# Kernel optimization log

Hardware: AMD Instinct MI355X
Metric: run time of the kernel (lower is better)

The kernel has to match this reference:

```python
import jax, jax.numpy as jnp
import numpy as np

B, D, T, K = 32, 64, 4096, 512
COMMITMENT_COST = 0.25


def setup_inputs() -> dict:
    key = jax.random.key(0)
    k1, k2 = jax.random.split(key)
    z = jax.random.normal(k1, (B, D, T), dtype=jnp.float32)
    # nn.Embedding init: uniform(-1/K, 1/K)
    codebook = jax.random.uniform(k2, (K, D), dtype=jnp.float32,
                                  minval=-1.0 / K, maxval=1.0 / K)
    return {"z": z, "codebook": codebook}


def reference(z, codebook):
    sg = jax.lax.stop_gradient
    zt = jnp.transpose(z, (0, 2, 1))            # [B, T, D]
    zf = zt.reshape(-1, D)                      # [N, D], N = B*T
    # squared L2 distances: ||z||^2 + ||e||^2 - 2 z.e  -> [N, K]
    dists = (jnp.sum(zf * zf, axis=1, keepdims=True)
             + jnp.sum(codebook * codebook, axis=1)
             - 2.0 * jnp.matmul(zf, codebook.T))
    idx = jnp.argmin(dists, axis=1)             # [N]
    # gather codebook rows (same math as one-hot @ codebook)
    quantized = codebook[idx].reshape(zt.shape)  # [B, T, D]
    codebook_loss = jnp.mean((sg(quantized) - zt) ** 2)
    commitment_loss = jnp.mean((quantized - sg(zt)) ** 2)
    vq_loss = codebook_loss + COMMITMENT_COST * commitment_loss
    # straight-through estimator
    quantized_st = zt + sg(quantized - zt)
    quantized_out = jnp.transpose(quantized_st, (0, 2, 1))  # [B, D, T]
    indices = idx.reshape(B, T)
    return vq_loss, quantized_out, indices
```

## Files before the change

### kernel.cpp

```cpp
#include <hip/hip_runtime.h>

#define NB 32
#define ND 64
#define NT 4096
#define NK 512
#define NGRID 1024

typedef __attribute__((ext_vector_type(8))) short short8;
typedef __attribute__((ext_vector_type(16))) float f32x16;
typedef unsigned int uint32;
typedef unsigned short ushort16_t;

#define PERM(r) ((((r) & 7) * 16) + ((r) >> 3))
#define STR 68
#define ESTR 66
#define MARGIN 4e-4f
#define RCAP 4

__device__ __forceinline__ ushort16_t bf16rne(float f) {
    uint32 u = __float_as_uint(f);
    return (ushort16_t)((u + 0x7FFFu + ((u >> 16) & 1u)) >> 16);
}
__device__ __forceinline__ float bf16tof(ushort16_t h) {
    return __uint_as_float(((uint32)h) << 16);
}

__global__ void prep_kernel(const float* __restrict__ cb,
                            uint4* __restrict__ cbfrag,
                            float* __restrict__ enorm,
                            double* __restrict__ loss_acc,
                            uint32* __restrict__ counter) {
    const int bi = blockIdx.x, tid = threadIdx.x;
    if (bi < 16) {
        const int t = bi * 256 + tid;
        const int c = t >> 8, rem = t & 255, s = rem >> 6, L = rem & 63;
        const int kcode = c * 32 + (L & 31);
        const int dbase = s * 16 + ((L >> 5) << 3);
        const float* src = cb + (size_t)kcode * 64 + dbase;
        const float4 pa = *(const float4*)src;
        const float4 pb = *(const float4*)(src + 4);
        const float f[8] = {pa.x, pa.y, pa.z, pa.w, pb.x, pb.y, pb.z, pb.w};
        uint32 hw[4], lw[4];
#pragma unroll
        for (int i = 0; i < 4; ++i) {
            const ushort16_t h0 = bf16rne(f[2*i]);
            const ushort16_t h1 = bf16rne(f[2*i+1]);
            const ushort16_t l0 = bf16rne(f[2*i]   - bf16tof(h0));
            const ushort16_t l1 = bf16rne(f[2*i+1] - bf16tof(h1));
            hw[i] = (uint32)h0 | ((uint32)h1 << 16);
            lw[i] = (uint32)l0 | ((uint32)l1 << 16);
        }
        cbfrag[(size_t)((c*4+s)*2 + 0)*64 + L] = make_uint4(hw[0],hw[1],hw[2],hw[3]);
        cbfrag[(size_t)((c*4+s)*2 + 1)*64 + L] = make_uint4(lw[0],lw[1],lw[2],lw[3]);
    } else {
        if (tid == 0) { *loss_acc = 0.0; *counter = 0u; }
        for (int k = tid; k < NK; k += 256) {
            const float* e = cb + (size_t)k * ND;
            float r[8];
#pragma unroll
            for (int j = 0; j < 8; ++j) {
                float s = __fmul_rn(e[j], e[j]);
#pragma unroll
                for (int i = 1; i < 8; ++i)
                    s = __fadd_rn(s, __fmul_rn(e[8*i+j], e[8*i+j]));
                r[j] = s;
            }
            enorm[k] = __fadd_rn(__fadd_rn(__fadd_rn(r[0],r[1]), __fadd_rn(r[2],r[3])),
                                 __fadd_rn(__fadd_rn(r[4],r[5]), __fadd_rn(r[6],r[7])));
        }
    }
}

__device__ __forceinline__ float exact_dist(const float* __restrict__ zrow,
                                            const float* __restrict__ cb,
                                            const float* __restrict__ enl,
                                            float zn, int k2) {
    const float4* e4 = (const float4*)(cb + (size_t)k2 * ND);
    float a = 0.0f;
#pragma unroll
    for (int w = 0; w < 16; ++w) {
        const float4 ev = e4[w];
        const float4 zv = *(const float4*)(zrow + 4 * w);
        a = __builtin_fmaf(zv.x, ev.x, a);
        a = __builtin_fmaf(zv.y, ev.y, a);
        a = __builtin_fmaf(zv.z, ev.z, a);
        a = __builtin_fmaf(zv.w, ev.w, a);
    }
    return __fsub_rn(__fadd_rn(zn, enl[k2]), __fmul_rn(2.0f, a));
}

__global__ __launch_bounds__(256, 3) void vq_main(const float* __restrict__ z,
                                                  const float* __restrict__ cb,
                                                  const uint4* __restrict__ cbfrag,
                                                  const float* __restrict__ enorm,
                                                  float* __restrict__ qout,
                                                  float* __restrict__ idxout,
                                                  double* __restrict__ loss_acc,
                                                  uint32* __restrict__ counter,
                                                  float* __restrict__ out0) {
    __shared__ __align__(16) char smem[46112];
    float*       zl   = (float*)smem;
    float*       enl  = (float*)(smem + 34816);
    float*       znl  = (float*)(smem + 36864);
    ushort16_t*  cand = (ushort16_t*)(smem + 37376);
    int*         sfin = (int*)(smem + 45568);
    double*      sred = (double*)(smem + 46080);

    const int bi    = blockIdx.x;
    const int b     = bi >> 5;
    const int tbase = (bi & 31) * 128;
    const int tid   = threadIdx.x;
    const size_t zoff = (size_t)b * (ND * NT) + tbase;

#pragma unroll
    for (int j = 0; j < 8; ++j) {
        const int qq = j * 256 + tid;
        const int i4 = qq & 31, d = qq >> 5;
        const float4 v = *(const float4*)(z + zoff + (size_t)d * NT + i4 * 4);
        const float vv[4] = {v.x, v.y, v.z, v.w};
#pragma unroll
        for (int c = 0; c < 4; ++c) {
            const int r = i4 * 4 + c;
            zl[PERM(r) * STR + d] = vv[c];
        }
    }
    for (int k = tid; k < NK; k += 256) enl[k] = enorm[k];
    __syncthreads();

    if (tid < 128) {
        const int r = tid;
        const float4* zr4 = (const float4*)&zl[PERM(r) * STR];
        float x[64];
#pragma unroll
        for (int wq = 0; wq < 16; ++wq) {
            const float4 t4 = zr4[wq];
            x[4*wq] = t4.x; x[4*wq+1] = t4.y; x[4*wq+2] = t4.z; x[4*wq+3] = t4.w;
        }
        float r8[8];
#pragma unroll
        for (int jj = 0; jj < 8; ++jj) {
            float s = __fmul_rn(x[jj], x[jj]);
#pragma unroll
            for (int ii = 1; ii < 8; ++ii)
                s = __fadd_rn(s, __fmul_rn(x[8*ii+jj], x[8*ii+jj]));
            r8[jj] = s;
        }
        znl[r] = __fadd_rn(__fadd_rn(__fadd_rn(r8[0],r8[1]), __fadd_rn(r8[2],r8[3])),
                           __fadd_rn(__fadd_rn(r8[4],r8[5]), __fadd_rn(r8[6],r8[7])));
    }

    const int L    = tid & 63;
    const int w    = tid >> 6;
    const int h    = L >> 5;
    const int rowl = w * 32 + (L & 31);
    short8 bhf[4], blf[4];
    {
        const float* zrow = &zl[PERM(rowl) * STR];
#pragma unroll
        for (int s = 0; s < 4; ++s) {
            const int d0 = s * 16 + h * 8;
            const float4 pa = *(const float4*)(zrow + d0);
            const float4 pb = *(const float4*)(zrow + d0 + 4);
            const float f[8] = {pa.x, pa.y, pa.z, pa.w, pb.x, pb.y, pb.z, pb.w};
            uint32 hw[4], lw[4];
#pragma unroll
            for (int i = 0; i < 4; ++i) {
                const ushort16_t h0 = bf16rne(f[2*i]);
                const ushort16_t h1 = bf16rne(f[2*i+1]);
                const ushort16_t l0 = bf16rne(f[2*i]   - bf16tof(h0));
                const ushort16_t l1 = bf16rne(f[2*i+1] - bf16tof(h1));
                hw[i] = (uint32)h0 | ((uint32)h1 << 16);
                lw[i] = (uint32)l0 | ((uint32)l1 << 16);
            }
            union { uint4 u; short8 s8; } uh, ul;
            uh.u = make_uint4(hw[0],hw[1],hw[2],hw[3]);
            ul.u = make_uint4(lw[0],lw[1],lw[2],lw[3]);
            bhf[s] = uh.s8; blf[s] = ul.s8;
        }
    }
    __syncthreads();

    float best  = __builtin_inff();
    int   bestk = 0;
    {
        uint4 buf0[8], buf1[8];
#pragma unroll
        for (int p = 0; p < 8; ++p) buf0[p] = cbfrag[(size_t)p * 64 + L];
#pragma unroll 2
        for (int c = 0; c < 16; ++c) {
            const uint4* cur = (c & 1) ? buf1 : buf0;
            uint4*       nxt = (c & 1) ? buf0 : buf1;
#pragma unroll
            for (int p = 0; p < 8; ++p)
                nxt[p] = cbfrag[(size_t)((c + 1) * 8 + p) * 64 + L];
            f32x16 acc;
#pragma unroll
            for (int r = 0; r < 16; ++r) acc[r] = 0.0f;
#pragma unroll
            for (int s = 0; s < 4; ++s) {
                union { uint4 u; short8 s8; } ah, al;
                ah.u = cur[s * 2 + 0];
                al.u = cur[s * 2 + 1];
                acc = __builtin_amdgcn_mfma_f32_32x32x16_bf16(ah.s8, bhf[s], acc, 0, 0, 0);
                acc = __builtin_amdgcn_mfma_f32_32x32x16_bf16(al.s8, bhf[s], acc, 0, 0, 0);
                acc = __builtin_amdgcn_mfma_f32_32x32x16_bf16(ah.s8, blf[s], acc, 0, 0, 0);
            }
#pragma unroll
            for (int r = 0; r < 16; ++r) {
                const int kc = c * 32 + ((r & 3) + 8 * (r >> 2) + 4 * h);
                const float sv = __builtin_fmaf(-2.0f, acc[r], enl[kc]);
                if (sv < best) { best = sv; bestk = kc; }
            }
        }
    }
    {
        const float ob  = __shfl_xor(best, 32);
        const int   obk = __shfl_xor(bestk, 32);
        if (ob < best || (ob == best && obk < bestk)) { best = ob; bestk = obk; }
    }
    const float thresh = best + MARGIN;

    int myc = 0, ovf = 0;
    ushort16_t* mylist = cand + (rowl * 2 + h) * RCAP;
    {
        uint4 buf0[8], buf1[8];
#pragma unroll
        for (int p = 0; p < 8; ++p) buf0[p] = cbfrag[(size_t)p * 64 + L];
#pragma unroll 2
        for (int c = 0; c < 16; ++c) {
            const uint4* cur = (c & 1) ? buf1 : buf0;
            uint4*       nxt = (c & 1) ? buf0 : buf1;
#pragma unroll
            for (int p = 0; p < 8; ++p)
                nxt[p] = cbfrag[(size_t)((c + 1) * 8 + p) * 64 + L];
            f32x16 acc;
#pragma unroll
            for (int r = 0; r < 16; ++r) acc[r] = 0.0f;
#pragma unroll
            for (int s = 0; s < 4; ++s) {
                union { uint4 u; short8 s8; } ah, al;
                ah.u = cur[s * 2 + 0];
                al.u = cur[s * 2 + 1];
                acc = __builtin_amdgcn_mfma_f32_32x32x16_bf16(ah.s8, bhf[s], acc, 0, 0, 0);
                acc = __builtin_amdgcn_mfma_f32_32x32x16_bf16(al.s8, bhf[s], acc, 0, 0, 0);
                acc = __builtin_amdgcn_mfma_f32_32x32x16_bf16(ah.s8, blf[s], acc, 0, 0, 0);
            }
#pragma unroll
            for (int r = 0; r < 16; ++r) {
                const int kc = c * 32 + ((r & 3) + 8 * (r >> 2) + 4 * h);
                const float sv = __builtin_fmaf(-2.0f, acc[r], enl[kc]);
                if (sv <= thresh && kc != bestk) {
                    if (myc < RCAP) mylist[myc++] = (ushort16_t)kc;
                    else ovf = 1;
                }
            }
        }
    }

    const float* zrow = &zl[PERM(rowl) * STR];
    const float  zn   = znl[rowl];
    const int    totr = myc + __shfl_xor(myc, 32);
    const int    aovf = ovf | __shfl_xor(ovf, 32);

    int bk;
    if (aovf) {
        float bd = __builtin_inff(); bk = 0x7FFFFFFF;
        for (int c = 0; c < 16; ++c)
#pragma unroll
            for (int qd = 0; qd < 4; ++qd)
#pragma unroll
                for (int i = 0; i < 4; ++i) {
                    const int k2 = c * 32 + qd * 8 + h * 4 + i;
                    const float dv = exact_dist(zrow, cb, enl, zn, k2);
                    if (dv < bd || (dv == bd && k2 < bk)) { bd = dv; bk = k2; }
                }
        const float obd = __shfl_xor(bd, 32);
        const int   obk = __shfl_xor(bk, 32);
        if (obd < bd || (obd == bd && obk < bk)) bk = obk;
    } else if (totr > 0) {
        float bd = __builtin_inff(); bk = 0x7FFFFFFF;
        if (((bestk >> 2) & 1) == h) {
            bd = exact_dist(zrow, cb, enl, zn, bestk);
            bk = bestk;
        }
        for (int i = 0; i < myc; ++i) {
            const int k2 = mylist[i];
            const float dv = exact_dist(zrow, cb, enl, zn, k2);
            if (dv < bd || (dv == bd && k2 < bk)) { bd = dv; bk = k2; }
        }
        const float obd = __shfl_xor(bd, 32);
        const int   obk = __shfl_xor(bk, 32);
        if (obd < bd || (obd == bd && obk < bk)) bk = obk;
    } else {
        bk = bestk;
    }
    if (h == 0) {
        sfin[rowl] = bk;
        idxout[(size_t)b * NT + tbase + rowl] = (float)bk;
    }
    __syncthreads();

    float* ech = zl;
#pragma unroll
    for (int j = 0; j < 8; ++j) {
        const int qq  = j * 256 + tid;
        const int row = qq >> 4, d4 = qq & 15;
        const float4 v = *(const float4*)(cb + (size_t)sfin[row] * ND + d4 * 4);
        float* dst = &ech[row * ESTR + d4 * 4];
        *(float2*)(dst)     = make_float2(v.x, v.y);
        *(float2*)(dst + 2) = make_float2(v.z, v.w);
    }
    __syncthreads();

    double lsum = 0.0;
#pragma unroll 4
    for (int j = 0; j < 32; ++j) {
        const int qq = j * 256 + tid;
        const int ir = qq & 127, d = qq >> 7;
        const float zv = z[zoff + (size_t)d * NT + ir];
        const float ev = ech[ir * ESTR + d];
        const float diff = __fsub_rn(ev, zv);
        qout[(size_t)b * (ND*NT) + (size_t)d * NT + tbase + ir] = __fadd_rn(zv, diff);
        lsum += (double)diff * (double)diff;
    }
#pragma unroll
    for (int off = 32; off > 0; off >>= 1) lsum += __shfl_down(lsum, off, 64);
    if ((tid & 63) == 0) sred[tid >> 6] = lsum;
    __syncthreads();

    if (tid == 0) {
        const double bsum = (sred[0] + sred[1]) + (sred[2] + sred[3]);
        atomicAdd(loss_acc, bsum);
        __threadfence();
        const uint32 old = atomicAdd(counter, 1u);
        if (old == (uint32)(NGRID - 1)) {
            __threadfence();
            const double tot = *(volatile double*)loss_acc;
            const double m = tot / (double)((size_t)NB * NT * ND);
            out0[0] = (float)(1.25 * m);
        }
    }
}

extern "C" void kernel_launch(void* const* d_in, const int* in_sizes, int n_in,
                              void* d_out, int out_size, void* d_ws, size_t ws_size,
                              hipStream_t stream) {
    const float* z  = (const float*)d_in[0];
    const float* cb = (const float*)d_in[1];

    float* out      = (float*)d_out;
    float* loss_out = out;
    float* qout     = out + 1;
    float* idxout   = out + 1 + (size_t)NB * ND * NT;

    uint4*  cbfrag   = (uint4*)d_ws;
    float*  enorm    = (float*)((char*)d_ws + 139264);
    double* loss_acc = (double*)((char*)d_ws + 141312);
    uint32* counter  = (uint32*)((char*)d_ws + 141320);

    prep_kernel<<<17, 256, 0, stream>>>(cb, cbfrag, enorm, loss_acc, counter);
    vq_main<<<NGRID, 256, 0, stream>>>(z, cb, cbfrag, enorm, qout, idxout,
                                       loss_acc, counter, loss_out);
}
```

Measured before the change: 201.1 us.

## Fuse candidate collection into single MFMA pass with register ring buffer

Removes the second full MFMA distance pass over the codebook. Near-best candidates are now tracked in a single pass, packed as quantized scores plus indices into a four-entry register shift buffer. This drops the shared-memory candidate list, shrinking LDS so launch bounds can target 4 blocks per SM. The cost is more branchy per-element logic, extra register pressure, and a possibly different overflow pattern that falls back to the exact full scan.

```diff
diff --git a/kernel.cpp b/kernel.cpp
--- a/kernel.cpp
+++ b/kernel.cpp
@@ -14,8 +14,7 @@
 #define PERM(r) ((((r) & 7) * 16) + ((r) >> 3))
 #define STR 68
 #define ESTR 66
-#define MARGIN 4e-4f
-#define RCAP 4
+#define M2 4e-4f
 
 __device__ __forceinline__ ushort16_t bf16rne(float f) {
     uint32 u = __float_as_uint(f);
@@ -89,7 +88,7 @@
     return __fsub_rn(__fadd_rn(zn, enl[k2]), __fmul_rn(2.0f, a));
 }
 
-__global__ __launch_bounds__(256, 3) void vq_main(const float* __restrict__ z,
+__global__ __launch_bounds__(256, 4) void vq_main(const float* __restrict__ z,
                                                   const float* __restrict__ cb,
                                                   const uint4* __restrict__ cbfrag,
                                                   const float* __restrict__ enorm,
@@ -98,13 +97,12 @@
                                                   double* __restrict__ loss_acc,
                                                   uint32* __restrict__ counter,
                                                   float* __restrict__ out0) {
-    __shared__ __align__(16) char smem[46112];
+    __shared__ __align__(16) char smem[37920];
     float*       zl   = (float*)smem;
     float*       enl  = (float*)(smem + 34816);
     float*       znl  = (float*)(smem + 36864);
-    ushort16_t*  cand = (ushort16_t*)(smem + 37376);
-    int*         sfin = (int*)(smem + 45568);
-    double*      sred = (double*)(smem + 46080);
+    int*         sfin = (int*)(smem + 37376);
+    double*      sred = (double*)(smem + 37888);
 
     const int bi    = blockIdx.x;
     const int b     = bi >> 5;
@@ -180,8 +178,12 @@
     }
     __syncthreads();
 
-    float best  = __builtin_inff();
-    int   bestk = 0;
+    float  bmax = -__builtin_inff();
+    int    bk   = 0;
+    float  thr  = -__builtin_inff();
+    uint32 thrq = 0xFFFFFFFFu;
+    uint32 r0 = 0u, r1 = 0u, r2 = 0u, r3 = 0u;
+    int    ovf  = 0;
     {
         uint4 buf0[8], buf1[8];
 #pragma unroll
@@ -207,64 +209,53 @@
             }
 #pragma unroll
             for (int r = 0; r < 16; ++r) {
-                const int kc = c * 32 + ((r & 3) + 8 * (r >> 2) + 4 * h);
-                const float sv = __builtin_fmaf(-2.0f, acc[r], enl[kc]);
-                if (sv < best) { best = sv; bestk = kc; }
-            }
-        }
-    }
-    {
-        const float ob  = __shfl_xor(best, 32);
-        const int   obk = __shfl_xor(bestk, 32);
-        if (ob < best || (ob == best && obk < bestk)) { best = ob; bestk = obk; }
-    }
-    const float thresh = best + MARGIN;
-
-    int myc = 0, ovf = 0;
-    ushort16_t* mylist = cand + (rowl * 2 + h) * RCAP;
-    {
-        uint4 buf0[8], buf1[8];
-#pragma unroll
-        for (int p = 0; p < 8; ++p) buf0[p] = cbfrag[(size_t)p * 64 + L];
-#pragma unroll 2
-        for (int c = 0; c < 16; ++c) {
-            const uint4* cur = (c & 1) ? buf1 : buf0;
-            uint4*       nxt = (c & 1) ? buf0 : buf1;
-#pragma unroll
-            for (int p = 0; p < 8; ++p)
-                nxt[p] = cbfrag[(size_t)((c + 1) * 8 + p) * 64 + L];
-            f32x16 acc;
-#pragma unroll
-            for (int r = 0; r < 16; ++r) acc[r] = 0.0f;
-#pragma unroll
-            for (int s = 0; s < 4; ++s) {
-                union { uint4 u; short8 s8; } ah, al;
-                ah.u = cur[s * 2 + 0];
-                al.u = cur[s * 2 + 1];
-                acc = __builtin_amdgcn_mfma_f32_32x32x16_bf16(ah.s8, bhf[s], acc, 0, 0, 0);
-                acc = __builtin_amdgcn_mfma_f32_32x32x16_bf16(al.s8, bhf[s], acc, 0, 0, 0);
-                acc = __builtin_amdgcn_mfma_f32_32x32x16_bf16(ah.s8, blf[s], acc, 0, 0, 0);
-            }
-#pragma unroll
-            for (int r = 0; r < 16; ++r) {
-                const int kc = c * 32 + ((r & 3) + 8 * (r >> 2) + 4 * h);
-                const float sv = __builtin_fmaf(-2.0f, acc[r], enl[kc]);
-                if (sv <= thresh && kc != bestk) {
-                    if (myc < RCAP) mylist[myc++] = (ushort16_t)kc;
-                    else ovf = 1;
+                const float a = acc[r];
+                if (a >= thr) {
+                    const int kc = c * 32 + ((r & 3) + 8 * (r >> 2) + 4 * h);
+                    if (a > bmax) {
+                        if (bmax >= a - M2) {
+                            const uint32 pv =
+                                (__float_as_uint(bmax + 0.5f) & ~0x1FFu) | (uint32)bk;
+                            ovf |= ((r3 & ~0x1FFu) >= thrq) ? 1 : 0;
+                            r3 = r2; r2 = r1; r1 = r0; r0 = pv;
+                        }
+                        bmax = a; bk = kc;
+                        thr  = a - M2;
+                        thrq = __float_as_uint(thr + 0.5f) & ~0x1FFu;
+                    } else {
+                        const uint32 pv =
+                            (__float_as_uint(a + 0.5f) & ~0x1FFu) | (uint32)kc;
+                        ovf |= ((r3 & ~0x1FFu) >= thrq) ? 1 : 0;
+                        r3 = r2; r2 = r1; r1 = r0; r0 = pv;
+                    }
                 }
             }
         }
     }
 
+    const float bmaxL = bmax;
+    const int   bkL   = bk;
+
+    {
+        const float ob  = __shfl_xor(bmax, 32);
+        const int   obk = __shfl_xor(bk, 32);
+        if (ob > bmax || (ob == bmax && obk < bk)) { bmax = ob; bk = obk; }
+    }
+    const float  thrf = bmax - M2;
+    const uint32 thrF = __float_as_uint(thrf + 0.5f) & ~0x1FFu;
+    const int lbRival = (bkL != bk) && (bmaxL >= thrf);
+    const int nriv = lbRival
+                   + (((r0 & ~0x1FFu) >= thrF) ? 1 : 0) + (((r1 & ~0x1FFu) >= thrF) ? 1 : 0)
+                   + (((r2 & ~0x1FFu) >= thrF) ? 1 : 0) + (((r3 & ~0x1FFu) >= thrF) ? 1 : 0);
+    const int totr = nriv + __shfl_xor(nriv, 32);
+    const int aovf = ovf | __shfl_xor(ovf, 32);
+
     const float* zrow = &zl[PERM(rowl) * STR];
     const float  zn   = znl[rowl];
-    const int    totr = myc + __shfl_xor(myc, 32);
-    const int    aovf = ovf | __shfl_xor(ovf, 32);
-
-    int bk;
+
+    int bkf;
     if (aovf) {
-        float bd = __builtin_inff(); bk = 0x7FFFFFFF;
+        float bd = __builtin_inff(); int bq = 0x7FFFFFFF;
         for (int c = 0; c < 16; ++c)
 #pragma unroll
             for (int qd = 0; qd < 4; ++qd)
@@ -272,31 +263,36 @@
                 for (int i = 0; i < 4; ++i) {
                     const int k2 = c * 32 + qd * 8 + h * 4 + i;
                     const float dv = exact_dist(zrow, cb, enl, zn, k2);
-                    if (dv < bd || (dv == bd && k2 < bk)) { bd = dv; bk = k2; }
+                    if (dv < bd || (dv == bd && k2 < bq)) { bd = dv; bq = k2; }
                 }
         const float obd = __shfl_xor(bd, 32);
-        const int   obk = __shfl_xor(bk, 32);
-        if (obd < bd || (obd == bd && obk < bk)) bk = obk;
+        const int   obq = __shfl_xor(bq, 32);
+        bkf = (obd < bd || (obd == bd && obq < bq)) ? obq : bq;
     } else if (totr > 0) {
-        float bd = __builtin_inff(); bk = 0x7FFFFFFF;
-        if (((bestk >> 2) & 1) == h) {
-            bd = exact_dist(zrow, cb, enl, zn, bestk);
-            bk = bestk;
-        }
-        for (int i = 0; i < myc; ++i) {
-            const int k2 = mylist[i];
-            const float dv = exact_dist(zrow, cb, enl, zn, k2);
-            if (dv < bd || (dv == bd && k2 < bk)) { bd = dv; bk = k2; }
-        }
+        float bd = __builtin_inff(); bkf = 0x7FFFFFFF;
+        if (((bk >> 2) & 1) == h) {
+            bd = exact_dist(zrow, cb, enl, zn, bk);
+            bkf = bk;
+        }
+        if (lbRival) {
+            const float dv = exact_dist(zrow, cb, enl, zn, bkL);
+            if (dv < bd || (dv == bd && bkL < bkf)) { bd = dv; bkf = bkL; }
+        }
+#define TRYC(ri) if (((ri) & ~0x1FFu) >= thrF) { \
+            const int k2 = (int)((ri) & 0x1FFu); \
+            const float dv = exact_dist(zrow, cb, enl, zn, k2); \
+            if (dv < bd || (dv == bd && k2 < bkf)) { bd = dv; bkf = k2; } }
+        TRYC(r0) TRYC(r1) TRYC(r2) TRYC(r3)
+#undef TRYC
         const float obd = __shfl_xor(bd, 32);
-        const int   obk = __shfl_xor(bk, 32);
-        if (obd < bd || (obd == bd && obk < bk)) bk = obk;
+        const int   obq = __shfl_xor(bkf, 32);
+        if (obd < bd || (obd == bd && obq < bkf)) bkf = obq;
     } else {
-        bk = bestk;
+        bkf = bk;
     }
     if (h == 0) {
-        sfin[rowl] = bk;
-        idxout[(size_t)b * NT + tbase + rowl] = (float)bk;
+        sfin[rowl] = bkf;
+        idxout[(size_t)b * NT + tbase + rowl] = (float)bkf;
     }
     __syncthreads();
 
```

Result: slower. 314.3 us (+56.3%).
